# Performance work log

Hardware: AMD Instinct MI355X
Metric: run time of the kernel (lower is better)

The kernel has to match this reference:

```python
import math
import jax, jax.numpy as jnp
import numpy as np

B, T, D, H = 4, 1024, 1024, 8
HD = D // H  # head_dim = 128

def _trigram_dirs():
    # 8 trigrams = all sign combinations in {−1,+1}^3, L2-normalized (p=2, dim=1)
    t = np.array([[(i >> b & 1) * 2 - 1 for b in (2, 1, 0)] for i in range(8)], dtype=np.float32)
    return jnp.asarray(t / np.linalg.norm(t, axis=1, keepdims=True))

def setup_inputs() -> dict:
    key = jax.random.key(0)
    k1, k2, k3, k4 = jax.random.split(key, 4)
    x = jax.random.normal(k1, (B, T, D), dtype=jnp.float32)
    Wqkv = jax.random.normal(k2, (D, 3 * D), dtype=jnp.float32) * 0.02
    Wout = jax.random.normal(k3, (D, D), dtype=jnp.float32) * 0.02
    # head_scales init to 0 in the module; use nonzero values so the geo-bias path is exercised
    head_scales = jax.random.normal(k4, (H,), dtype=jnp.float32) * 0.1
    head_dirs = _trigram_dirs()  # [H, 3] buffer
    return {"x": x, "Wqkv": Wqkv, "Wout": Wout, "head_scales": head_scales, "head_dirs": head_dirs}

def reference(x, Wqkv, Wout, head_scales, head_dirs):
    b, t, d = x.shape
    scale = 1.0 / math.sqrt(HD)
    qkv = (x @ Wqkv).reshape(b, t, 3, H, HD)
    qkv = jnp.transpose(qkv, (2, 0, 3, 1, 4))  # [3, B, H, T, HD]
    q, k, v = qkv[0], qkv[1], qkv[2]
    # scores: [B, H, T, T]
    scores = jnp.einsum('bhqd,bhkd->bhqk', q, k) * scale
    # rank-1 trigram geometric bias from first 3 dims of q/k
    q_proj = jnp.einsum('bhtd,hd->bht', q[..., :3], head_dirs)
    k_proj = jnp.einsum('bhtd,hd->bht', k[..., :3], head_dirs)
    geo_bias = q_proj[..., :, None] * k_proj[..., None, :]  # [B, H, T, T]
    scores = scores + head_scales[None, :, None, None] * geo_bias
    causal = jnp.tril(jnp.ones((t, t), dtype=bool))
    scores = jnp.where(causal, scores, -jnp.inf)
    attn = jax.nn.softmax(scores, axis=-1)
    out = jnp.einsum('bhqk,bhkd->bhqd', attn, v)  # [B, H, T, HD]
    out = jnp.transpose(out, (0, 2, 1, 3)).reshape(b, t, d)
    return out @ Wout
```

## Files before the change

kernel.cpp:

```cpp
#include <hip/hip_runtime.h>
#include <stdint.h>

typedef __attribute__((ext_vector_type(8))) short short8;
typedef __attribute__((ext_vector_type(4))) short short4v;
typedef __attribute__((ext_vector_type(4))) float f32x4;

__device__ __forceinline__ short f2bf(float x) {
  union { float f; uint32_t u; } c; c.f = x;
  uint32_t r = (c.u + 0x7FFFu + ((c.u >> 16) & 1u)) >> 16;
  return (short)r;
}
__device__ __forceinline__ float b2f(short s) {
  union { uint32_t u; float f; } c; c.u = ((uint32_t)(uint16_t)s) << 16;
  return c.f;
}
__device__ __forceinline__ uint32_t pack2bf(float lo, float hi) {
  return ((uint32_t)(uint16_t)f2bf(hi) << 16) | (uint32_t)(uint16_t)f2bf(lo);
}

__global__ __launch_bounds__(256) void prep_kernel(const float* __restrict__ x,
                                                   const float* __restrict__ Wqkv,
                                                   const float* __restrict__ Wout,
                                                   short* __restrict__ xb,
                                                   short* __restrict__ wqkvT,
                                                   short* __restrict__ woutT) {
  __shared__ __align__(16) short tile[32][33];
  const int bid = blockIdx.x;
  if (bid < 2048) {
    const int n4 = (4 * 1024 * 1024) / 4;
    int i = bid * 256 + threadIdx.x;
    for (; i < n4; i += 2048 * 256) {
      float4 v = reinterpret_cast<const float4*>(x)[i];
      short4v o;
      o.x = f2bf(v.x); o.y = f2bf(v.y); o.z = f2bf(v.z); o.w = f2bf(v.w);
      reinterpret_cast<short4v*>(xb)[i] = o;
    }
  } else {
    const float* in;
    short* out;
    int K, N, bx, by;
    if (bid < 2048 + 3072) {
      const int idx = bid - 2048;
      in = Wqkv; out = wqkvT; K = 1024; N = 3072; bx = idx % 96; by = idx / 96;
    } else {
      const int idx = bid - 5120;
      in = Wout; out = woutT; K = 1024; N = 1024; bx = idx % 32; by = idx / 32;
    }
    const int nb = bx * 32, kb = by * 32;
    const int tx = threadIdx.x & 31, ty = threadIdx.x >> 5;
#pragma unroll
    for (int i = 0; i < 32; i += 8)
      tile[ty + i][tx] = f2bf(in[(size_t)(kb + ty + i) * N + nb + tx]);
    __syncthreads();
#pragma unroll
    for (int i = 0; i < 32; i += 8)
      out[(size_t)(nb + ty + i) * K + kb + tx] = tile[tx][ty + i];
  }
}

__global__ __launch_bounds__(256) void vtrans_kernel(const short* __restrict__ qkvb,
                                                     short* __restrict__ vT) {
  __shared__ __align__(16) short tile[64][65];
  const int bid = blockIdx.x;
  const int b = bid / 256;
  const int kv0 = (bid % 16) * 64, c0 = ((bid / 16) % 16) * 64;
  const int tx = threadIdx.x & 15, ty = threadIdx.x >> 4;
  const short* src = qkvb + (size_t)(b * 1024) * 3072 + 2048;
#pragma unroll
  for (int i = 0; i < 64; i += 16) {
    int r = ty + i;
#pragma unroll
    for (int j = 0; j < 4; ++j)
      tile[r][tx * 4 + j] = src[(size_t)(kv0 + r) * 3072 + c0 + tx * 4 + j];
  }
  __syncthreads();
  short* dst = vT + (size_t)b * 1024 * 1024;
#pragma unroll
  for (int i = 0; i < 64; i += 16) {
    int cc = ty + i;
#pragma unroll
    for (int j = 0; j < 4; ++j)
      dst[(size_t)(c0 + cc) * 1024 + kv0 + tx * 4 + j] = tile[tx * 4 + j][cc];
  }
}

template <int OUT_BF16>
__global__ __launch_bounds__(256) void gemm_kernel(const short* __restrict__ A,
                                                   const short* __restrict__ Bt,
                                                   void* __restrict__ Cout,
                                                   int K, int ldc) {
  __shared__ __align__(16) short Al[2][128 * 32];
  __shared__ __align__(16) short Bl[2][128 * 32];
  const int t = threadIdx.x;
  const int lane = t & 63, w = t >> 6;
  const int wr = w >> 1, wc = w & 1;
  const int g = lane >> 4, c16 = lane & 15;
  const int wg = blockIdx.x;
  const int xcd = wg & 7, ii = wg >> 3;
  const int bx = (xcd & 1) * 12 + (ii % 12);
  const int by = (xcd >> 1) * 8 + (ii / 12);
  const int row0 = by * 128, col0 = bx * 128;

  f32x4 acc[4][4];
#pragma unroll
  for (int m = 0; m < 4; ++m)
#pragma unroll
    for (int n = 0; n < 4; ++n) {
      f32x4 z = {0.0f, 0.0f, 0.0f, 0.0f};
      acc[m][n] = z;
    }

  auto stage = [&](int buf, int kt) {
    const int k0 = kt * 32;
#pragma unroll
    for (int i = 0; i < 2; ++i) {
      const int qb = i * 256 + (t & 192);
      const int q = qb + lane;
      const int r = q >> 2;
      const int c = (q & 3) ^ ((r >> 1) & 3);
      const short* ga = A + (size_t)(row0 + r) * K + k0 + c * 8;
      const short* gb = Bt + (size_t)(col0 + r) * K + k0 + c * 8;
      __builtin_amdgcn_global_load_lds((const __attribute__((address_space(1))) void*)ga,
                                       (__attribute__((address_space(3))) void*)&Al[buf][qb * 8],
                                       16, 0, 0);
      __builtin_amdgcn_global_load_lds((const __attribute__((address_space(1))) void*)gb,
                                       (__attribute__((address_space(3))) void*)&Bl[buf][qb * 8],
                                       16, 0, 0);
    }
  };

  stage(0, 0);
  __syncthreads();
  const int NK = K >> 5;
  int cur = 0;
  const int rA0 = wr * 64 + c16;
  const int rB0 = wc * 64 + c16;
  for (int kt = 0; kt < NK; ++kt) {
    if (kt + 1 < NK) stage(cur ^ 1, kt + 1);
    short8 aF[4], bF[4];
#pragma unroll
    for (int m = 0; m < 4; ++m) {
      const int r = rA0 + m * 16;
      const int c = g ^ ((r >> 1) & 3);
      aF[m] = *reinterpret_cast<const short8*>(&Al[cur][r * 32 + c * 8]);
    }
#pragma unroll
    for (int n = 0; n < 4; ++n) {
      const int r = rB0 + n * 16;
      const int c = g ^ ((r >> 1) & 3);
      bF[n] = *reinterpret_cast<const short8*>(&Bl[cur][r * 32 + c * 8]);
    }
#pragma unroll
    for (int m = 0; m < 4; ++m)
#pragma unroll
      for (int n = 0; n < 4; ++n)
        acc[m][n] = __builtin_amdgcn_mfma_f32_16x16x32_bf16(aF[m], bF[n], acc[m][n], 0, 0, 0);
    __syncthreads();
    cur ^= 1;
  }

  const int er = row0 + wr * 64 + g * 4;
  const int ec = col0 + wc * 64 + c16;
#pragma unroll
  for (int m = 0; m < 4; ++m)
#pragma unroll
    for (int n = 0; n < 4; ++n)
#pragma unroll
      for (int j = 0; j < 4; ++j) {
        const size_t off = (size_t)(er + m * 16 + j) * ldc + ec + n * 16;
        if (OUT_BF16)
          ((short*)Cout)[off] = f2bf(acc[m][n][j]);
        else
          ((float*)Cout)[off] = acc[m][n][j];
      }
}

template <int OUT_BF16>
__global__ __launch_bounds__(256) void gemm64_kernel(const short* __restrict__ A,
                                                     const short* __restrict__ Bt,
                                                     void* __restrict__ Cout,
                                                     int K, int ldc) {
  __shared__ __align__(16) short Al[2][128 * 32];
  __shared__ __align__(16) short Bl[2][64 * 32];
  const int t = threadIdx.x;
  const int lane = t & 63, w = t >> 6;
  const int wr = w >> 1, wc = w & 1;
  const int g = lane >> 4, c16 = lane & 15;
  const int row0 = blockIdx.y * 128, col0 = blockIdx.x * 64;

  f32x4 acc[4][2];
#pragma unroll
  for (int m = 0; m < 4; ++m)
#pragma unroll
    for (int n = 0; n < 2; ++n) {
      f32x4 z = {0.0f, 0.0f, 0.0f, 0.0f};
      acc[m][n] = z;
    }

  auto stage = [&](int buf, int kt) {
    const int k0 = kt * 32;
#pragma unroll
    for (int i = 0; i < 2; ++i) {
      const int qb = i * 256 + (t & 192);
      const int q = qb + lane;
      const int r = q >> 2;
      const int c = (q & 3) ^ ((r >> 1) & 3);
      const short* ga = A + (size_t)(row0 + r) * K + k0 + c * 8;
      __builtin_amdgcn_global_load_lds((const __attribute__((address_space(1))) void*)ga,
                                       (__attribute__((address_space(3))) void*)&Al[buf][qb * 8],
                                       16, 0, 0);
    }
    {
      const int qb = (t & 192);
      const int q = qb + lane;
      const int r = q >> 2;
      const int c = (q & 3) ^ ((r >> 1) & 3);
      const short* gb = Bt + (size_t)(col0 + r) * K + k0 + c * 8;
      __builtin_amdgcn_global_load_lds((const __attribute__((address_space(1))) void*)gb,
                                       (__attribute__((address_space(3))) void*)&Bl[buf][qb * 8],
                                       16, 0, 0);
    }
  };

  stage(0, 0);
  __syncthreads();
  const int NK = K >> 5;
  int cur = 0;
  const int rA0 = wr * 64 + c16;
  const int rB0 = wc * 32 + c16;
  for (int kt = 0; kt < NK; ++kt) {
    if (kt + 1 < NK) stage(cur ^ 1, kt + 1);
    short8 aF[4], bF[2];
#pragma unroll
    for (int m = 0; m < 4; ++m) {
      const int r = rA0 + m * 16;
      const int c = g ^ ((r >> 1) & 3);
      aF[m] = *reinterpret_cast<const short8*>(&Al[cur][r * 32 + c * 8]);
    }
#pragma unroll
    for (int n = 0; n < 2; ++n) {
      const int r = rB0 + n * 16;
      const int c = g ^ ((r >> 1) & 3);
      bF[n] = *reinterpret_cast<const short8*>(&Bl[cur][r * 32 + c * 8]);
    }
#pragma unroll
    for (int m = 0; m < 4; ++m)
#pragma unroll
      for (int n = 0; n < 2; ++n)
        acc[m][n] = __builtin_amdgcn_mfma_f32_16x16x32_bf16(aF[m], bF[n], acc[m][n], 0, 0, 0);
    __syncthreads();
    cur ^= 1;
  }

  const int er = row0 + wr * 64 + g * 4;
  const int ec = col0 + wc * 32 + c16;
#pragma unroll
  for (int m = 0; m < 4; ++m)
#pragma unroll
    for (int n = 0; n < 2; ++n)
#pragma unroll
      for (int j = 0; j < 4; ++j) {
        const size_t off = (size_t)(er + m * 16 + j) * ldc + ec + n * 16;
        if (OUT_BF16)
          ((short*)Cout)[off] = f2bf(acc[m][n][j]);
        else
          ((float*)Cout)[off] = acc[m][n][j];
      }
}

__global__ __launch_bounds__(256) void attn_kernel(const short* __restrict__ qkvb,
                                                   const short* __restrict__ vT,
                                                   const float* __restrict__ head_scales,
                                                   const float* __restrict__ hdirs,
                                                   short* __restrict__ attnb) {
  __shared__ __align__(16) short Kl[2][64 * 128];
  __shared__ __align__(16) short Vl[2][128 * 64];
  __shared__ float kp_lds[2][64];

  const int bid = blockIdx.x;
  const int bh = (bid & 7) * 4 + ((bid >> 3) & 3);
  const int r2 = bid >> 5;
  const int qt = (bid < 256) ? (15 - r2) : (r2 - 8);
  const int b = bh >> 3, h = bh & 7;
  const int t = threadIdx.x, lane = t & 63, w = t >> 6;
  const int g = lane >> 4, c16 = lane & 15;
  const int q0w = qt * 64 + w * 16;
  const int q_abs = q0w + c16;

  const short* qbase = qkvb + (size_t)(b * 1024) * 3072 + h * 128;
  const short* kbase = qbase + 1024;
  const short* vtb = vT + (size_t)bh * 128 * 1024;

  const float LOG2E = 1.44269504088896f;
  const float scale2 = 0.08838834764831845f * 1.44269504088896f;
  const float d0 = hdirs[h * 3], d1 = hdirs[h * 3 + 1], d2 = hdirs[h * 3 + 2];

  short8 aQ[4];
  float hqp;
  {
    const short* qr = qbase + (size_t)(q0w + c16) * 3072;
#pragma unroll
    for (int kk = 0; kk < 4; ++kk)
      aQ[kk] = *reinterpret_cast<const short8*>(qr + kk * 32 + g * 8);
    const float hs = head_scales[h];
    hqp = hs * LOG2E * (b2f(qr[0]) * d0 + b2f(qr[1]) * d1 + b2f(qr[2]) * d2);
  }

  float m_s = -1e30f, l_s = 0.0f;
  f32x4 accO[8];
#pragma unroll
  for (int d = 0; d < 8; ++d) {
    f32x4 z = {0.0f, 0.0f, 0.0f, 0.0f};
    accO[d] = z;
  }

  auto stageKV = [&](int buf, int kvt) {
    const int kv0 = kvt * 64;
#pragma unroll
    for (int i = 0; i < 4; ++i) {
      const int s = w * 4 + i;
      {
        const int r = s * 4 + g;
        const int c = c16 ^ (r & 7);
        const short* ga = kbase + (size_t)(kv0 + r) * 3072 + c * 8;
        __builtin_amdgcn_global_load_lds((const __attribute__((address_space(1))) void*)ga,
                                         (__attribute__((address_space(3))) void*)&Kl[buf][s * 512],
                                         16, 0, 0);
      }
      {
        const int r = s * 8 + (lane >> 3);
        const int c = (lane & 7) ^ (r & 7);
        const short* ga = vtb + (size_t)r * 1024 + kv0 + c * 8;
        __builtin_amdgcn_global_load_lds((const __attribute__((address_space(1))) void*)ga,
                                         (__attribute__((address_space(3))) void*)&Vl[buf][s * 512],
                                         16, 0, 0);
      }
    }
    if (lane < 16) {
      const short* kr = kbase + (size_t)(kv0 + w * 16 + lane) * 3072;
      kp_lds[buf][w * 16 + lane] = b2f(kr[0]) * d0 + b2f(kr[1]) * d1 + b2f(kr[2]) * d2;
    }
  };

  const int nkv = qt + 1;
  stageKV(0, 0);
  __syncthreads();
  int cur = 0;
  for (int kvt = 0; kvt < nkv; ++kvt) {
    const int kv0 = kvt * 64;
    if (kvt + 1 < nkv) stageKV(cur ^ 1, kvt + 1);
    const short* Kc = Kl[cur];
    const short* Vc = Vl[cur];
    const float* kpc = kp_lds[cur];
    const bool diag = (kvt == qt);
    const int nmax = diag ? (w + 1) : 4;

    float p[4][4];
#pragma unroll
    for (int n = 0; n < 4; ++n) {
      if (n >= nmax) {
        p[n][0] = -1e30f; p[n][1] = -1e30f; p[n][2] = -1e30f; p[n][3] = -1e30f;
        continue;
      }
      f32x4 s4 = {0.0f, 0.0f, 0.0f, 0.0f};
      const int r = n * 16 + c16;
#pragma unroll
      for (int kk = 0; kk < 4; ++kk) {
        const int cch = (kk * 4 + g) ^ (r & 7);
        short8 bK = *reinterpret_cast<const short8*>(&Kc[r * 128 + cch * 8]);
        s4 = __builtin_amdgcn_mfma_f32_16x16x32_bf16(bK, aQ[kk], s4, 0, 0, 0);
      }
      if (diag) {
#pragma unroll
        for (int j = 0; j < 4; ++j) {
          const int kloc = n * 16 + g * 4 + j;
          const float v = s4[j] * scale2 + hqp * kpc[kloc];
          p[n][j] = (kv0 + kloc <= q_abs) ? v : -1e30f;
        }
      } else {
#pragma unroll
        for (int j = 0; j < 4; ++j) {
          const int kloc = n * 16 + g * 4 + j;
          p[n][j] = s4[j] * scale2 + hqp * kpc[kloc];
        }
      }
    }

    float mx;
    {
      float a0 = fmaxf(fmaxf(p[0][0], p[0][1]), fmaxf(p[0][2], p[0][3]));
      float a1 = fmaxf(fmaxf(p[1][0], p[1][1]), fmaxf(p[1][2], p[1][3]));
      float a2 = fmaxf(fmaxf(p[2][0], p[2][1]), fmaxf(p[2][2], p[2][3]));
      float a3 = fmaxf(fmaxf(p[3][0], p[3][1]), fmaxf(p[3][2], p[3][3]));
      mx = fmaxf(fmaxf(a0, a1), fmaxf(a2, a3));
      mx = fmaxf(mx, __shfl_xor(mx, 16, 64));
      mx = fmaxf(mx, __shfl_xor(mx, 32, 64));
    }

    if (__any(mx - m_s > 11.54f)) {
      const float mn = fmaxf(m_s, mx);
      const float alpha = exp2f(m_s - mn);
      m_s = mn;
      l_s *= alpha;
      float aO[4];
#pragma unroll
      for (int j = 0; j < 4; ++j) aO[j] = __shfl(alpha, g * 4 + j, 64);
#pragma unroll
      for (int d = 0; d < 8; ++d)
#pragma unroll
        for (int j = 0; j < 4; ++j) accO[d][j] *= aO[j];
    }

    float s01 = 0.0f, s23 = 0.0f;
#pragma unroll
    for (int n = 0; n < 4; ++n) {
      if (n >= nmax) {
        p[n][0] = 0.0f; p[n][1] = 0.0f; p[n][2] = 0.0f; p[n][3] = 0.0f;
        continue;
      }
      float e0 = exp2f(p[n][0] - m_s), e1 = exp2f(p[n][1] - m_s);
      float e2 = exp2f(p[n][2] - m_s), e3 = exp2f(p[n][3] - m_s);
      p[n][0] = e0; p[n][1] = e1; p[n][2] = e2; p[n][3] = e3;
      if (n < 2) s01 += (e0 + e1) + (e2 + e3); else s23 += (e0 + e1) + (e2 + e3);
    }
    float sum = s01 + s23;
    sum += __shfl_xor(sum, 16, 64);
    sum += __shfl_xor(sum, 32, 64);
    l_s += sum;

    uint32_t pk[4][2];
#pragma unroll
    for (int n = 0; n < 4; ++n) {
      pk[n][0] = pack2bf(p[n][0], p[n][1]);
      pk[n][1] = pack2bf(p[n][2], p[n][3]);
    }

    const int kkmax = (nmax <= 2) ? 1 : 2;

    union { uint32_t d[4]; short8 s; } aPu[2];
#pragma unroll
    for (int kk = 0; kk < 2; ++kk) {
      if (kk >= kkmax) continue;
#pragma unroll
      for (int wd = 0; wd < 4; ++wd) {
        const int src = (2 * (g & 1) + (wd >> 1)) * 16 + c16;
        const uint32_t v0 = (uint32_t)__shfl((int)pk[kk * 2][wd & 1], src, 64);
        const uint32_t v1 = (uint32_t)__shfl((int)pk[kk * 2 + 1][wd & 1], src, 64);
        aPu[kk].d[wd] = (g >= 2) ? v1 : v0;
      }
    }

    if (kkmax == 2) {
#pragma unroll
      for (int dt = 0; dt < 8; ++dt) {
        const int r = dt * 16 + c16;
        const int c0x = (g) ^ (r & 7);
        const int c1x = (4 + g) ^ (r & 7);
        short8 bV0 = *reinterpret_cast<const short8*>(&Vc[r * 64 + c0x * 8]);
        short8 bV1 = *reinterpret_cast<const short8*>(&Vc[r * 64 + c1x * 8]);
        accO[dt] = __builtin_amdgcn_mfma_f32_16x16x32_bf16(aPu[0].s, bV0, accO[dt], 0, 0, 0);
        accO[dt] = __builtin_amdgcn_mfma_f32_16x16x32_bf16(aPu[1].s, bV1, accO[dt], 0, 0, 0);
      }
    } else {
#pragma unroll
      for (int dt = 0; dt < 8; ++dt) {
        const int r = dt * 16 + c16;
        const int c0x = (g) ^ (r & 7);
        short8 bV0 = *reinterpret_cast<const short8*>(&Vc[r * 64 + c0x * 8]);
        accO[dt] = __builtin_amdgcn_mfma_f32_16x16x32_bf16(aPu[0].s, bV0, accO[dt], 0, 0, 0);
      }
    }
    __syncthreads();
    cur ^= 1;
  }

  float linv[4];
#pragma unroll
  for (int j = 0; j < 4; ++j) linv[j] = 1.0f / __shfl(l_s, g * 4 + j, 64);
#pragma unroll
  for (int j = 0; j < 4; ++j) {
    const size_t rowoff = (size_t)(b * 1024 + q0w + g * 4 + j) * 1024 + h * 128;
#pragma unroll
    for (int dt = 0; dt < 8; ++dt)
      attnb[rowoff + dt * 16 + c16] = f2bf(accO[dt][j] * linv[j]);
  }
}

extern "C" void kernel_launch(void* const* d_in, const int* in_sizes, int n_in,
                              void* d_out, int out_size, void* d_ws, size_t ws_size,
                              hipStream_t stream) {
  const float* x = (const float*)d_in[0];
  const float* Wqkv = (const float*)d_in[1];
  const float* Wout = (const float*)d_in[2];
  const float* hscale = (const float*)d_in[3];
  const float* hdirs = (const float*)d_in[4];
  float* out = (float*)d_out;

  char* ws = (char*)d_ws;
  short* xb = (short*)(ws);
  short* wqkvT = (short*)(ws + (size_t)8 * 1024 * 1024);
  short* woutT = (short*)(ws + (size_t)14 * 1024 * 1024);
  short* qkvb = (short*)(ws + (size_t)16 * 1024 * 1024);
  short* vT = (short*)(ws + (size_t)40 * 1024 * 1024);
  short* attnb = (short*)(ws + (size_t)48 * 1024 * 1024);

  prep_kernel<<<6144, 256, 0, stream>>>(x, Wqkv, Wout, xb, wqkvT, woutT);
  gemm_kernel<1><<<768, 256, 0, stream>>>(xb, wqkvT, (void*)qkvb, 1024, 3072);
  vtrans_kernel<<<1024, 256, 0, stream>>>(qkvb, vT);
  attn_kernel<<<512, 256, 0, stream>>>(qkvb, vT, hscale, hdirs, attnb);
  gemm64_kernel<0><<<dim3(16, 32), 256, 0, stream>>>(attnb, woutT, out, 1024, 1024);
}
```

Before: 107.6 us.

## Fuse V transpose into QKV GEMM epilogue and remap output GEMM blocks per XCD

The QKV projection GEMM now writes its V tiles transposed straight into the vT buffer. It stages each tile through a swizzled LDS region that reuses the staging buffers via a union, which removes the separate vtrans kernel launch and its extra global read and write of V. The output GEMM moves from a 2D grid to a 1D grid with an XCD-aware block mapping, so row blocks sharing A stay on the same XCD for L2 reuse. The V-tile epilogue adds an extra __syncthreads and LDS round trip for those blocks.

```diff
diff --git a/kernel.cpp b/kernel.cpp
--- a/kernel.cpp
+++ b/kernel.cpp
@@ -58,39 +58,15 @@
   }
 }
 
-__global__ __launch_bounds__(256) void vtrans_kernel(const short* __restrict__ qkvb,
-                                                     short* __restrict__ vT) {
-  __shared__ __align__(16) short tile[64][65];
-  const int bid = blockIdx.x;
-  const int b = bid / 256;
-  const int kv0 = (bid % 16) * 64, c0 = ((bid / 16) % 16) * 64;
-  const int tx = threadIdx.x & 15, ty = threadIdx.x >> 4;
-  const short* src = qkvb + (size_t)(b * 1024) * 3072 + 2048;
-#pragma unroll
-  for (int i = 0; i < 64; i += 16) {
-    int r = ty + i;
-#pragma unroll
-    for (int j = 0; j < 4; ++j)
-      tile[r][tx * 4 + j] = src[(size_t)(kv0 + r) * 3072 + c0 + tx * 4 + j];
-  }
-  __syncthreads();
-  short* dst = vT + (size_t)b * 1024 * 1024;
-#pragma unroll
-  for (int i = 0; i < 64; i += 16) {
-    int cc = ty + i;
-#pragma unroll
-    for (int j = 0; j < 4; ++j)
-      dst[(size_t)(c0 + cc) * 1024 + kv0 + tx * 4 + j] = tile[tx * 4 + j][cc];
-  }
-}
-
-template <int OUT_BF16>
 __global__ __launch_bounds__(256) void gemm_kernel(const short* __restrict__ A,
                                                    const short* __restrict__ Bt,
-                                                   void* __restrict__ Cout,
+                                                   short* __restrict__ Cout,
+                                                   short* __restrict__ vTout,
                                                    int K, int ldc) {
-  __shared__ __align__(16) short Al[2][128 * 32];
-  __shared__ __align__(16) short Bl[2][128 * 32];
+  __shared__ __align__(16) union {
+    struct { short Al[2][128 * 32]; short Bl[2][128 * 32]; } g;
+    short T[128 * 128];
+  } sm;
   const int t = threadIdx.x;
   const int lane = t & 63, w = t >> 6;
   const int wr = w >> 1, wc = w & 1;
@@ -121,10 +97,10 @@
       const short* ga = A + (size_t)(row0 + r) * K + k0 + c * 8;
       const short* gb = Bt + (size_t)(col0 + r) * K + k0 + c * 8;
       __builtin_amdgcn_global_load_lds((const __attribute__((address_space(1))) void*)ga,
-                                       (__attribute__((address_space(3))) void*)&Al[buf][qb * 8],
+                                       (__attribute__((address_space(3))) void*)&sm.g.Al[buf][qb * 8],
                                        16, 0, 0);
       __builtin_amdgcn_global_load_lds((const __attribute__((address_space(1))) void*)gb,
-                                       (__attribute__((address_space(3))) void*)&Bl[buf][qb * 8],
+                                       (__attribute__((address_space(3))) void*)&sm.g.Bl[buf][qb * 8],
                                        16, 0, 0);
     }
   };
@@ -142,13 +118,13 @@
     for (int m = 0; m < 4; ++m) {
       const int r = rA0 + m * 16;
       const int c = g ^ ((r >> 1) & 3);
-      aF[m] = *reinterpret_cast<const short8*>(&Al[cur][r * 32 + c * 8]);
+      aF[m] = *reinterpret_cast<const short8*>(&sm.g.Al[cur][r * 32 + c * 8]);
     }
 #pragma unroll
     for (int n = 0; n < 4; ++n) {
       const int r = rB0 + n * 16;
       const int c = g ^ ((r >> 1) & 3);
-      bF[n] = *reinterpret_cast<const short8*>(&Bl[cur][r * 32 + c * 8]);
+      bF[n] = *reinterpret_cast<const short8*>(&sm.g.Bl[cur][r * 32 + c * 8]);
     }
 #pragma unroll
     for (int m = 0; m < 4; ++m)
@@ -159,20 +135,43 @@
     cur ^= 1;
   }
 
-  const int er = row0 + wr * 64 + g * 4;
-  const int ec = col0 + wc * 64 + c16;
-#pragma unroll
-  for (int m = 0; m < 4; ++m)
-#pragma unroll
-    for (int n = 0; n < 4; ++n)
-#pragma unroll
-      for (int j = 0; j < 4; ++j) {
-        const size_t off = (size_t)(er + m * 16 + j) * ldc + ec + n * 16;
-        if (OUT_BF16)
-          ((short*)Cout)[off] = f2bf(acc[m][n][j]);
-        else
-          ((float*)Cout)[off] = acc[m][n][j];
-      }
+  if (col0 < 2048) {
+    const int er = row0 + wr * 64 + g * 4;
+    const int ec = col0 + wc * 64 + c16;
+#pragma unroll
+    for (int m = 0; m < 4; ++m)
+#pragma unroll
+      for (int n = 0; n < 4; ++n)
+#pragma unroll
+        for (int j = 0; j < 4; ++j)
+          Cout[(size_t)(er + m * 16 + j) * ldc + ec + n * 16] = f2bf(acc[m][n][j]);
+  } else {
+#pragma unroll
+    for (int m = 0; m < 4; ++m) {
+      const int t128 = wr * 64 + m * 16 + g * 4;
+      const int chunk = t128 >> 3, half = (t128 >> 2) & 1;
+#pragma unroll
+      for (int n = 0; n < 4; ++n) {
+        const int c128 = wc * 64 + n * 16 + c16;
+        short4v v4;
+        v4.x = f2bf(acc[m][n][0]); v4.y = f2bf(acc[m][n][1]);
+        v4.z = f2bf(acc[m][n][2]); v4.w = f2bf(acc[m][n][3]);
+        const int off = c128 * 128 + ((chunk ^ (c128 & 7)) << 3) + half * 4;
+        *reinterpret_cast<short4v*>(&sm.T[off]) = v4;
+      }
+    }
+    __syncthreads();
+    const int b = by >> 3, tt0 = (by & 7) * 128;
+    const int cv0 = col0 - 2048;
+    short* dst = vTout + (size_t)b * 1024 * 1024 + tt0;
+#pragma unroll
+    for (int it = 0; it < 8; ++it) {
+      const int idx = it * 256 + t;
+      const int row = idx >> 4, seg = idx & 15;
+      short8 v = *reinterpret_cast<const short8*>(&sm.T[row * 128 + ((seg ^ (row & 7)) << 3)]);
+      *reinterpret_cast<short8*>(&dst[(size_t)(cv0 + row) * 1024 + seg * 8]) = v;
+    }
+  }
 }
 
 template <int OUT_BF16>
@@ -186,7 +185,11 @@
   const int lane = t & 63, w = t >> 6;
   const int wr = w >> 1, wc = w & 1;
   const int g = lane >> 4, c16 = lane & 15;
-  const int row0 = blockIdx.y * 128, col0 = blockIdx.x * 64;
+  const int wg = blockIdx.x;
+  const int xcd = wg & 7, ii = wg >> 3;
+  const int by = xcd * 4 + (ii >> 4);
+  const int bx = ii & 15;
+  const int row0 = by * 128, col0 = bx * 64;
 
   f32x4 acc[4][2];
 #pragma unroll
@@ -505,8 +508,7 @@
   short* attnb = (short*)(ws + (size_t)48 * 1024 * 1024);
 
   prep_kernel<<<6144, 256, 0, stream>>>(x, Wqkv, Wout, xb, wqkvT, woutT);
-  gemm_kernel<1><<<768, 256, 0, stream>>>(xb, wqkvT, (void*)qkvb, 1024, 3072);
-  vtrans_kernel<<<1024, 256, 0, stream>>>(qkvb, vT);
+  gemm_kernel<<<768, 256, 0, stream>>>(xb, wqkvT, qkvb, vT, 1024, 3072);
   attn_kernel<<<512, 256, 0, stream>>>(qkvb, vT, hscale, hdirs, attnb);
-  gemm64_kernel<0><<<dim3(16, 32), 256, 0, stream>>>(attnb, woutT, out, 1024, 1024);
-}
+  gemm64_kernel<0><<<512, 256, 0, stream>>>(attnb, woutT, out, 1024, 1024);
+}
```

Result: faster. 98.68 us (-8.3%).
